# Performance work log

Hardware: AMD Instinct MI355X
Metric: run time of the kernel (lower is better)

Reference implementation:

```python
import jax, jax.numpy as jnp
import numpy as np

EPS_COS = 1e-8
EPS_SHARP = 1e-16


def setup_inputs() -> dict:
    key = jax.random.key(0)
    k1, k2, k3, k4 = jax.random.split(key, 4)
    B, H, R, C, M = 512, 512, 2048, 64, 3
    out_dim = 3 * C + 2 * M + 4  # 202
    h = jax.random.normal(k1, (B, H), dtype=jnp.float32)
    prev_w = jax.random.uniform(k2, (B, R), dtype=jnp.float32)
    prev_w = prev_w / prev_w.sum(axis=1, keepdims=True)  # valid focus distribution
    memory = jax.random.normal(k3, (B, R, C), dtype=jnp.float32)
    fc_w = jax.random.normal(k4, (out_dim, H), dtype=jnp.float32) * 0.05
    fc_b = jnp.zeros((out_dim,), dtype=jnp.float32)
    return {"h": h, "prev_w": prev_w, "memory": memory, "fc_w": fc_w, "fc_b": fc_b}


def _write_head(h, prev_w, memory, fc_w, fc_b):
    B, R, C = memory.shape
    total = fc_w.shape[0]
    shift_len = total - 3 * C - 3          # 2*max_shift + 1
    m = (shift_len - 1) // 2               # max_shift

    z = h @ fc_w.T + fc_b                  # [B, total]
    sizes = [C, 1, 1, shift_len, 1, C, C]
    offs = np.cumsum([0] + sizes)
    k     = jnp.tanh(z[:, offs[0]:offs[1]])                 # [B, C]
    beta  = jax.nn.softplus(z[:, offs[1]:offs[2]])          # [B, 1]
    g     = jax.nn.sigmoid(z[:, offs[2]:offs[3]])           # [B, 1]
    s     = jax.nn.softmax(z[:, offs[3]:offs[4]], axis=1)   # [B, 2m+1]
    gamma = jax.nn.softplus(z[:, offs[4]:offs[5]]) + 1.0    # [B, 1]
    e     = jax.nn.sigmoid(z[:, offs[5]:offs[6]])           # [B, C]
    a     = jnp.tanh(z[:, offs[6]:offs[7]])                 # [B, C]

    # content addressing: cosine similarity of k vs each memory row
    num = jnp.einsum('bc,brc->br', k, memory)
    k_n = jnp.maximum(jnp.linalg.norm(k, axis=1, keepdims=True), EPS_COS)   # [B,1]
    m_n = jnp.maximum(jnp.linalg.norm(memory, axis=2), EPS_COS)             # [B,R]
    w_c = jax.nn.softmax(beta * (num / (k_n * m_n)), axis=1)                # [B,R]

    # gated interpolation
    w_g = g * w_c + (1.0 - g) * prev_w                                      # [B,R]

    # circular shift (per-sample cross-correlation, O(B*R*(2m+1)))
    unrolled = jnp.concatenate([w_g[:, -m:], w_g, w_g[:, :m]], axis=1)      # [B, R+2m]
    windows = jnp.stack([unrolled[:, j:j + R] for j in range(2 * m + 1)], axis=1)  # [B,2m+1,R]
    w_s = jnp.einsum('bjr,bj->br', windows, s)                              # [B,R]

    # sharpen
    w_p = jnp.power(w_s, gamma)
    w = w_p / (w_p.sum(axis=1, keepdims=True) + EPS_SHARP)                  # [B,R]

    # erase + write (fused)
    wE = w[:, :, None]                                                      # [B,R,1]
    new_mem = memory * (1.0 - wE * e[:, None, :]) + wE * a[:, None, :]      # [B,R,C]
    return w, new_mem


def reference(h, prev_w, memory, fc_w, fc_b):
    return _write_head(h, prev_w, memory, fc_w, fc_b)
```

## Files before the change

kernel.cpp:

```cpp
#include <hip/hip_runtime.h>
#include <math.h>

#define BB 512
#define HH 512
#define RR 2048
#define CC 64
#define OUTD 202
#define PSTRIDE 208
#define K_OFF 0
#define E_OFF 64
#define A_OFF 128
#define S_OFF 192
#define COMBO_OFF 199
#define G_OFF 200
#define GAMMA_OFF 201

typedef float f32x4 __attribute__((ext_vector_type(4)));

__device__ __forceinline__ float softplusf_(float x) {
    return (x > 20.f) ? x : log1pf(expf(x));
}
__device__ __forceinline__ float sigmoidf_(float x) {
    return 1.f / (1.f + expf(-x));
}

__global__ __launch_bounds__(256) void params_kernel(
    const float* __restrict__ h, const float* __restrict__ fc_w,
    const float* __restrict__ fc_b, float* __restrict__ pw)
{
    __shared__ float h_sh[8][HH];
    __shared__ float z_sh[8][204];
    const int tid = threadIdx.x;
    const int b0 = blockIdx.x * 8;

    for (int idx = tid; idx < 8 * HH; idx += 256) {
        int j = idx >> 9, i = idx & 511;
        h_sh[j][i] = h[(size_t)(b0 + j) * HH + i];
    }
    __syncthreads();

    if (tid < OUTD) {
        float acc[8];
        #pragma unroll
        for (int j = 0; j < 8; ++j) acc[j] = 0.f;
        const float4* wr4 = (const float4*)(fc_w + (size_t)tid * HH);
        for (int i4 = 0; i4 < HH / 4; ++i4) {
            float4 wv = wr4[i4];
            int i = i4 * 4;
            #pragma unroll
            for (int j = 0; j < 8; ++j) {
                acc[j] = fmaf(wv.x, h_sh[j][i + 0], acc[j]);
                acc[j] = fmaf(wv.y, h_sh[j][i + 1], acc[j]);
                acc[j] = fmaf(wv.z, h_sh[j][i + 2], acc[j]);
                acc[j] = fmaf(wv.w, h_sh[j][i + 3], acc[j]);
            }
        }
        float bias = fc_b[tid];
        #pragma unroll
        for (int j = 0; j < 8; ++j) z_sh[j][tid] = acc[j] + bias;
    }
    __syncthreads();

    for (int idx = tid; idx < 8 * OUTD; idx += 256) {
        int j = idx / OUTD;
        int t = idx - j * OUTD;
        float z = z_sh[j][t];
        float* p = pw + (size_t)(b0 + j) * PSTRIDE;
        if (t < 64)            p[K_OFF + t] = tanhf(z);
        else if (t == 65)      p[G_OFF] = sigmoidf_(z);
        else if (t == 73)      p[GAMMA_OFF] = softplusf_(z) + 1.f;
        else if (t >= 74 && t < 138) p[E_OFF + (t - 74)] = sigmoidf_(z);
        else if (t >= 138)     p[A_OFF + (t - 138)] = tanhf(z);
    }
    __syncthreads();

    if (tid < 8) {
        int j = tid;
        float* p = pw + (size_t)(b0 + j) * PSTRIDE;
        float ss = 0.f;
        for (int c = 0; c < 64; ++c) {
            float kv = tanhf(z_sh[j][c]);
            ss += kv * kv;
        }
        float kn = fmaxf(sqrtf(ss), 1e-8f);
        float beta = softplusf_(z_sh[j][64]);
        p[COMBO_OFF] = beta / kn;
        float mx = -1e30f;
        for (int q = 0; q < 7; ++q) mx = fmaxf(mx, z_sh[j][66 + q]);
        float ev[7], se = 0.f;
        for (int q = 0; q < 7; ++q) { ev[q] = expf(z_sh[j][66 + q] - mx); se += ev[q]; }
        float inv = 1.f / se;
        for (int q = 0; q < 7; ++q) p[S_OFF + q] = ev[q] * inv;
    }
}

__global__ __launch_bounds__(256) void score_kernel(
    const float* __restrict__ memory, const float* __restrict__ pw,
    float* __restrict__ sc)
{
    const int tid = threadIdx.x;
    const int b = blockIdx.x >> 2;
    const int rbase = (blockIdx.x & 3) * 512;
    const int lane16 = tid & 15;
    const int rgrp = tid >> 4;
    const float* p = pw + (size_t)b * PSTRIDE;
    const float4 k4 = *(const float4*)(p + K_OFF + lane16 * 4);
    const float combo = p[COMBO_OFF];
    const float* memb = memory + (size_t)b * RR * CC;

    #pragma unroll 8
    for (int i = 0; i < 32; ++i) {
        int r = rbase + i * 16 + rgrp;
        float4 m4 = *(const float4*)(memb + (size_t)r * CC + lane16 * 4);
        float num = m4.x * k4.x + m4.y * k4.y + m4.z * k4.z + m4.w * k4.w;
        float ssq = m4.x * m4.x + m4.y * m4.y + m4.z * m4.z + m4.w * m4.w;
        #pragma unroll
        for (int m = 1; m < 16; m <<= 1) {
            num += __shfl_xor(num, m, 64);
            ssq += __shfl_xor(ssq, m, 64);
        }
        if (lane16 == 0) {
            float mn = fmaxf(sqrtf(ssq), 1e-8f);
            sc[(size_t)b * RR + r] = __expf(combo * num / mn);
        }
    }
}

__device__ __forceinline__ float block_reduce_sum256(float v, float* red) {
    #pragma unroll
    for (int m = 1; m < 64; m <<= 1) v += __shfl_xor(v, m, 64);
    int wid = threadIdx.x >> 6;
    if ((threadIdx.x & 63) == 0) red[wid] = v;
    __syncthreads();
    float x = red[0] + red[1] + red[2] + red[3];
    __syncthreads();
    return x;
}

__global__ __launch_bounds__(256) void weight_kernel(
    const float* __restrict__ sc, const float* __restrict__ prev_w,
    const float* __restrict__ pw, float* __restrict__ out_w)
{
    __shared__ float buf[RR];
    __shared__ float wg[RR];
    __shared__ float red[4];
    const int b = blockIdx.x;
    const int tid = threadIdx.x;
    const float* p = pw + (size_t)b * PSTRIDE;
    const float g = p[G_OFF];
    const float gamma = p[GAMMA_OFF];
    const float s0 = p[S_OFF + 0], s1 = p[S_OFF + 1], s2 = p[S_OFF + 2],
                s3 = p[S_OFF + 3], s4 = p[S_OFF + 4], s5 = p[S_OFF + 5],
                s6 = p[S_OFF + 6];

    float ls = 0.f;
    for (int r = tid; r < RR; r += 256) {
        float ev = sc[(size_t)b * RR + r];
        buf[r] = ev;
        ls += ev;
    }
    const float se = block_reduce_sum256(ls, red);
    const float invse = 1.f / se;

    for (int r = tid; r < RR; r += 256) {
        wg[r] = g * (buf[r] * invse) + (1.f - g) * prev_w[(size_t)b * RR + r];
    }
    __syncthreads();

    float lp = 0.f;
    for (int r = tid; r < RR; r += 256) {
        float acc = s0 * wg[(r - 3) & (RR - 1)]
                  + s1 * wg[(r - 2) & (RR - 1)]
                  + s2 * wg[(r - 1) & (RR - 1)]
                  + s3 * wg[r]
                  + s4 * wg[(r + 1) & (RR - 1)]
                  + s5 * wg[(r + 2) & (RR - 1)]
                  + s6 * wg[(r + 3) & (RR - 1)];
        float wp = __powf(acc, gamma);
        buf[r] = wp;
        lp += wp;
    }
    const float ps = block_reduce_sum256(lp, red);
    const float invp = 1.f / (ps + 1e-16f);

    for (int r = tid; r < RR; r += 256) {
        out_w[(size_t)b * RR + r] = buf[r] * invp;
    }
}

__global__ __launch_bounds__(256) void update_kernel(
    const float* __restrict__ memory, const float* __restrict__ w,
    const float* __restrict__ pw, float* __restrict__ out_mem)
{
    const int bid = (int)gridDim.x - 1 - (int)blockIdx.x;
    const int b = bid >> 2;
    const int rbase = (bid & 3) * 512;
    const int tid = threadIdx.x;
    const int lane16 = tid & 15;
    const int rgrp = tid >> 4;
    const float* p = pw + (size_t)b * PSTRIDE;
    const f32x4 e4 = *(const f32x4*)(p + E_OFF + lane16 * 4);
    const f32x4 a4 = *(const f32x4*)(p + A_OFF + lane16 * 4);
    const float* memb = memory + (size_t)b * RR * CC;
    float* omb = out_mem + (size_t)b * RR * CC;
    const float* wb = w + (size_t)b * RR;

    #pragma unroll 8
    for (int i = 0; i < 32; ++i) {
        int r = rbase + i * 16 + rgrp;
        float wv = wb[r];
        const f32x4* mp = (const f32x4*)(memb + (size_t)r * CC) + lane16;
        f32x4 m4 = __builtin_nontemporal_load(mp);
        f32x4 o;
        o.x = m4.x * (1.f - wv * e4.x) + wv * a4.x;
        o.y = m4.y * (1.f - wv * e4.y) + wv * a4.y;
        o.z = m4.z * (1.f - wv * e4.z) + wv * a4.z;
        o.w = m4.w * (1.f - wv * e4.w) + wv * a4.w;
        __builtin_nontemporal_store(o, (f32x4*)(omb + (size_t)r * CC) + lane16);
    }
}

extern "C" void kernel_launch(void* const* d_in, const int* in_sizes, int n_in,
                              void* d_out, int out_size, void* d_ws, size_t ws_size,
                              hipStream_t stream) {
    const float* h      = (const float*)d_in[0];
    const float* prev_w = (const float*)d_in[1];
    const float* memory = (const float*)d_in[2];
    const float* fc_w   = (const float*)d_in[3];
    const float* fc_b   = (const float*)d_in[4];

    float* pw      = (float*)d_ws;
    float* out_w   = (float*)d_out;
    float* out_mem = out_w + (size_t)BB * RR;
    float* sc      = out_mem;

    params_kernel<<<64, 256, 0, stream>>>(h, fc_w, fc_b, pw);
    score_kernel<<<BB * 4, 256, 0, stream>>>(memory, pw, sc);
    weight_kernel<<<BB, 256, 0, stream>>>(sc, prev_w, pw, out_w);
    update_kernel<<<BB * 4, 256, 0, stream>>>(memory, out_w, pw, out_mem);
}
```

Measured before the change: 199.1 us.

## Fuse weight normalization and memory update into one 1024-thread kernel per batch

Merges the weight computation and the erase/write memory update into a single kernel with one 1024-thread block per batch row. The final weights stay in shared memory for the update instead of being re-read from global, and one launch is removed. Scores now live in workspace rather than aliasing the output, with the old three-kernel path kept as a fallback when workspace is too small. The trade-off is that the 512 MB-scale memory update now runs on only 512 blocks, which may cut the parallelism available for the bandwidth-bound stream.

```diff
diff --git a/kernel.cpp b/kernel.cpp
--- a/kernel.cpp
+++ b/kernel.cpp
@@ -126,25 +126,34 @@
     }
 }
 
-__device__ __forceinline__ float block_reduce_sum256(float v, float* red) {
+__device__ __forceinline__ float block_reduce_sum16(float v, float* red) {
     #pragma unroll
     for (int m = 1; m < 64; m <<= 1) v += __shfl_xor(v, m, 64);
     int wid = threadIdx.x >> 6;
     if ((threadIdx.x & 63) == 0) red[wid] = v;
     __syncthreads();
-    float x = red[0] + red[1] + red[2] + red[3];
-    __syncthreads();
-    return x;
-}
-
-__global__ __launch_bounds__(256) void weight_kernel(
-    const float* __restrict__ sc, const float* __restrict__ prev_w,
-    const float* __restrict__ pw, float* __restrict__ out_w)
+    if (threadIdx.x < 16) {
+        float x = red[threadIdx.x];
+        #pragma unroll
+        for (int m = 1; m < 16; m <<= 1) x += __shfl_xor(x, m, 64);
+        if (threadIdx.x == 0) red[0] = x;
+    }
+    __syncthreads();
+    float r = red[0];
+    __syncthreads();
+    return r;
+}
+
+__global__ __launch_bounds__(1024) void weight_update_kernel(
+    const float* __restrict__ memory, const float* __restrict__ sc,
+    const float* __restrict__ prev_w, const float* __restrict__ pw,
+    float* __restrict__ out_w, float* __restrict__ out_mem)
 {
     __shared__ float buf[RR];
     __shared__ float wg[RR];
-    __shared__ float red[4];
-    const int b = blockIdx.x;
+    __shared__ float red[16];
+
+    const int b = (int)gridDim.x - 1 - (int)blockIdx.x;
     const int tid = threadIdx.x;
     const float* p = pw + (size_t)b * PSTRIDE;
     const float g = p[G_OFF];
@@ -154,12 +163,98 @@
                 s6 = p[S_OFF + 6];
 
     float ls = 0.f;
+    for (int r = tid; r < RR; r += 1024) {
+        float ev = sc[(size_t)b * RR + r];
+        buf[r] = ev;
+        ls += ev;
+    }
+    const float se = block_reduce_sum16(ls, red);
+    const float invse = 1.f / se;
+
+    for (int r = tid; r < RR; r += 1024) {
+        wg[r] = g * (buf[r] * invse) + (1.f - g) * prev_w[(size_t)b * RR + r];
+    }
+    __syncthreads();
+
+    float lp = 0.f;
+    for (int r = tid; r < RR; r += 1024) {
+        float acc = s0 * wg[(r - 3) & (RR - 1)]
+                  + s1 * wg[(r - 2) & (RR - 1)]
+                  + s2 * wg[(r - 1) & (RR - 1)]
+                  + s3 * wg[r]
+                  + s4 * wg[(r + 1) & (RR - 1)]
+                  + s5 * wg[(r + 2) & (RR - 1)]
+                  + s6 * wg[(r + 3) & (RR - 1)];
+        float wp = __powf(acc, gamma);
+        buf[r] = wp;
+        lp += wp;
+    }
+    const float ps = block_reduce_sum16(lp, red);
+    const float invp = 1.f / (ps + 1e-16f);
+
+    for (int r = tid; r < RR; r += 1024) {
+        float wv = buf[r] * invp;
+        wg[r] = wv;
+        __builtin_nontemporal_store(wv, out_w + (size_t)b * RR + r);
+    }
+    __syncthreads();
+
+    const int lane16 = tid & 15;
+    const int rgrp = tid >> 4;
+    const f32x4 e4 = *(const f32x4*)(p + E_OFF + lane16 * 4);
+    const f32x4 a4 = *(const f32x4*)(p + A_OFF + lane16 * 4);
+    const float* memb = memory + (size_t)b * RR * CC;
+    float* omb = out_mem + (size_t)b * RR * CC;
+
+    #pragma unroll 8
+    for (int i = 0; i < 32; ++i) {
+        int r = i * 64 + rgrp;
+        float wv = wg[r];
+        f32x4 m4 = __builtin_nontemporal_load(
+            (const f32x4*)(memb + (size_t)r * CC) + lane16);
+        f32x4 o;
+        o.x = m4.x * (1.f - wv * e4.x) + wv * a4.x;
+        o.y = m4.y * (1.f - wv * e4.y) + wv * a4.y;
+        o.z = m4.z * (1.f - wv * e4.z) + wv * a4.z;
+        o.w = m4.w * (1.f - wv * e4.w) + wv * a4.w;
+        __builtin_nontemporal_store(o, (f32x4*)(omb + (size_t)r * CC) + lane16);
+    }
+}
+
+__device__ __forceinline__ float block_reduce_sum4(float v, float* red) {
+    #pragma unroll
+    for (int m = 1; m < 64; m <<= 1) v += __shfl_xor(v, m, 64);
+    int wid = threadIdx.x >> 6;
+    if ((threadIdx.x & 63) == 0) red[wid] = v;
+    __syncthreads();
+    float x = red[0] + red[1] + red[2] + red[3];
+    __syncthreads();
+    return x;
+}
+
+__global__ __launch_bounds__(256) void weight_kernel(
+    const float* __restrict__ sc, const float* __restrict__ prev_w,
+    const float* __restrict__ pw, float* __restrict__ out_w)
+{
+    __shared__ float buf[RR];
+    __shared__ float wg[RR];
+    __shared__ float red[4];
+    const int b = blockIdx.x;
+    const int tid = threadIdx.x;
+    const float* p = pw + (size_t)b * PSTRIDE;
+    const float g = p[G_OFF];
+    const float gamma = p[GAMMA_OFF];
+    const float s0 = p[S_OFF + 0], s1 = p[S_OFF + 1], s2 = p[S_OFF + 2],
+                s3 = p[S_OFF + 3], s4 = p[S_OFF + 4], s5 = p[S_OFF + 5],
+                s6 = p[S_OFF + 6];
+
+    float ls = 0.f;
     for (int r = tid; r < RR; r += 256) {
         float ev = sc[(size_t)b * RR + r];
         buf[r] = ev;
         ls += ev;
     }
-    const float se = block_reduce_sum256(ls, red);
+    const float se = block_reduce_sum4(ls, red);
     const float invse = 1.f / se;
 
     for (int r = tid; r < RR; r += 256) {
@@ -180,7 +275,7 @@
         buf[r] = wp;
         lp += wp;
     }
-    const float ps = block_reduce_sum256(lp, red);
+    const float ps = block_reduce_sum4(lp, red);
     const float invp = 1.f / (ps + 1e-16f);
 
     for (int r = tid; r < RR; r += 256) {
@@ -209,8 +304,8 @@
     for (int i = 0; i < 32; ++i) {
         int r = rbase + i * 16 + rgrp;
         float wv = wb[r];
-        const f32x4* mp = (const f32x4*)(memb + (size_t)r * CC) + lane16;
-        f32x4 m4 = __builtin_nontemporal_load(mp);
+        f32x4 m4 = __builtin_nontemporal_load(
+            (const f32x4*)(memb + (size_t)r * CC) + lane16);
         f32x4 o;
         o.x = m4.x * (1.f - wv * e4.x) + wv * a4.x;
         o.y = m4.y * (1.f - wv * e4.y) + wv * a4.y;
@@ -232,10 +327,21 @@
     float* pw      = (float*)d_ws;
     float* out_w   = (float*)d_out;
     float* out_mem = out_w + (size_t)BB * RR;
-    float* sc      = out_mem;
+
+    const size_t pw_bytes = (size_t)BB * PSTRIDE * sizeof(float);
+    const size_t sc_bytes = (size_t)BB * RR * sizeof(float);
 
     params_kernel<<<64, 256, 0, stream>>>(h, fc_w, fc_b, pw);
-    score_kernel<<<BB * 4, 256, 0, stream>>>(memory, pw, sc);
-    weight_kernel<<<BB, 256, 0, stream>>>(sc, prev_w, pw, out_w);
-    update_kernel<<<BB * 4, 256, 0, stream>>>(memory, out_w, pw, out_mem);
-}
+
+    if (ws_size >= pw_bytes + sc_bytes) {
+        float* sc = pw + (size_t)BB * PSTRIDE;
+        score_kernel<<<BB * 4, 256, 0, stream>>>(memory, pw, sc);
+        weight_update_kernel<<<BB, 1024, 0, stream>>>(
+            memory, sc, prev_w, pw, out_w, out_mem);
+    } else {
+        float* sc = out_mem;
+        score_kernel<<<BB * 4, 256, 0, stream>>>(memory, pw, sc);
+        weight_kernel<<<BB, 256, 0, stream>>>(sc, prev_w, pw, out_w);
+        update_kernel<<<BB * 4, 256, 0, stream>>>(memory, out_w, pw, out_mem);
+    }
+}
```

After: 193.5 us. 1.03x faster.

## Chunk score/weight/update pipeline over batch halves for cache reuse of memory

Applied to the files above, without the earlier changes.

Splits the score, weight and update kernels into two batch chunks launched in sequence, and keeps the score buffer in workspace instead of the output. Each chunk's slice of the memory tensor is read by score and then again by update soon after, so the second read can hit the last-level cache instead of HBM. It adds kernel launches, drops the previous reverse block ordering in update, and falls back to the old path if the workspace is too small.

```diff
diff --git a/kernel.cpp b/kernel.cpp
--- a/kernel.cpp
+++ b/kernel.cpp
@@ -14,6 +14,9 @@
 #define COMBO_OFF 199
 #define G_OFF 200
 #define GAMMA_OFF 201
+
+#define NCHUNK 2
+#define CB (BB / NCHUNK)
 
 typedef float f32x4 __attribute__((ext_vector_type(4)));
 
@@ -96,10 +99,10 @@
 
 __global__ __launch_bounds__(256) void score_kernel(
     const float* __restrict__ memory, const float* __restrict__ pw,
-    float* __restrict__ sc)
-{
-    const int tid = threadIdx.x;
-    const int b = blockIdx.x >> 2;
+    float* __restrict__ sc, int bofs)
+{
+    const int tid = threadIdx.x;
+    const int b = bofs + (blockIdx.x >> 2);
     const int rbase = (blockIdx.x & 3) * 512;
     const int lane16 = tid & 15;
     const int rgrp = tid >> 4;
@@ -126,7 +129,7 @@
     }
 }
 
-__device__ __forceinline__ float block_reduce_sum256(float v, float* red) {
+__device__ __forceinline__ float block_reduce_sum4(float v, float* red) {
     #pragma unroll
     for (int m = 1; m < 64; m <<= 1) v += __shfl_xor(v, m, 64);
     int wid = threadIdx.x >> 6;
@@ -139,12 +142,12 @@
 
 __global__ __launch_bounds__(256) void weight_kernel(
     const float* __restrict__ sc, const float* __restrict__ prev_w,
-    const float* __restrict__ pw, float* __restrict__ out_w)
+    const float* __restrict__ pw, float* __restrict__ out_w, int bofs)
 {
     __shared__ float buf[RR];
     __shared__ float wg[RR];
     __shared__ float red[4];
-    const int b = blockIdx.x;
+    const int b = bofs + blockIdx.x;
     const int tid = threadIdx.x;
     const float* p = pw + (size_t)b * PSTRIDE;
     const float g = p[G_OFF];
@@ -159,7 +162,7 @@
         buf[r] = ev;
         ls += ev;
     }
-    const float se = block_reduce_sum256(ls, red);
+    const float se = block_reduce_sum4(ls, red);
     const float invse = 1.f / se;
 
     for (int r = tid; r < RR; r += 256) {
@@ -180,7 +183,7 @@
         buf[r] = wp;
         lp += wp;
     }
-    const float ps = block_reduce_sum256(lp, red);
+    const float ps = block_reduce_sum4(lp, red);
     const float invp = 1.f / (ps + 1e-16f);
 
     for (int r = tid; r < RR; r += 256) {
@@ -190,11 +193,10 @@
 
 __global__ __launch_bounds__(256) void update_kernel(
     const float* __restrict__ memory, const float* __restrict__ w,
-    const float* __restrict__ pw, float* __restrict__ out_mem)
-{
-    const int bid = (int)gridDim.x - 1 - (int)blockIdx.x;
-    const int b = bid >> 2;
-    const int rbase = (bid & 3) * 512;
+    const float* __restrict__ pw, float* __restrict__ out_mem, int bofs)
+{
+    const int b = bofs + ((int)blockIdx.x >> 2);
+    const int rbase = ((int)blockIdx.x & 3) * 512;
     const int tid = threadIdx.x;
     const int lane16 = tid & 15;
     const int rgrp = tid >> 4;
@@ -209,8 +211,8 @@
     for (int i = 0; i < 32; ++i) {
         int r = rbase + i * 16 + rgrp;
         float wv = wb[r];
-        const f32x4* mp = (const f32x4*)(memb + (size_t)r * CC) + lane16;
-        f32x4 m4 = __builtin_nontemporal_load(mp);
+        f32x4 m4 = __builtin_nontemporal_load(
+            (const f32x4*)(memb + (size_t)r * CC) + lane16);
         f32x4 o;
         o.x = m4.x * (1.f - wv * e4.x) + wv * a4.x;
         o.y = m4.y * (1.f - wv * e4.y) + wv * a4.y;
@@ -232,10 +234,25 @@
     float* pw      = (float*)d_ws;
     float* out_w   = (float*)d_out;
     float* out_mem = out_w + (size_t)BB * RR;
-    float* sc      = out_mem;
+
+    const size_t pw_bytes = (size_t)BB * PSTRIDE * sizeof(float);
+    const size_t sc_bytes = (size_t)BB * RR * sizeof(float);
 
     params_kernel<<<64, 256, 0, stream>>>(h, fc_w, fc_b, pw);
-    score_kernel<<<BB * 4, 256, 0, stream>>>(memory, pw, sc);
-    weight_kernel<<<BB, 256, 0, stream>>>(sc, prev_w, pw, out_w);
-    update_kernel<<<BB * 4, 256, 0, stream>>>(memory, out_w, pw, out_mem);
-}
+
+    if (ws_size >= pw_bytes + sc_bytes) {
+        float* sc = pw + (size_t)BB * PSTRIDE;
+        for (int c = 0; c < NCHUNK; ++c) {
+            int b0 = c * CB;
+            score_kernel<<<CB * 4, 256, 0, stream>>>(memory, pw, sc, b0);
+            weight_kernel<<<CB, 256, 0, stream>>>(sc, prev_w, pw, out_w, b0);
+            update_kernel<<<CB * 4, 256, 0, stream>>>(memory, out_w, pw,
+                                                      out_mem, b0);
+        }
+    } else {
+        float* sc = out_mem;
+        score_kernel<<<BB * 4, 256, 0, stream>>>(memory, pw, sc, 0);
+        weight_kernel<<<BB, 256, 0, stream>>>(sc, prev_w, pw, out_w, 0);
+        update_kernel<<<BB * 4, 256, 0, stream>>>(memory, out_w, pw, out_mem, 0);
+    }
+}
```

Result: slower. 215.8 us (+8.4%).

## Split softmax and shift stage across four blocks per sample via partial sums

Applied to the files above, without the earlier changes.

The score kernel now also emits per-block partial sums of the exponentiated scores. The single-block-per-sample weight kernel is replaced by a four-blocks-per-sample convolution kernel that loads a halo tile, applies the gated interpolation and circular shift, and writes un-normalized sharpened weights plus partial sums. The update kernel then applies the final normalization, writes the output weights and updates memory; its memory read is now a plain load instead of a nontemporal one. This path needs a larger workspace, and the old three-kernel path is kept as a fallback when the workspace is too small.

```diff
diff --git a/kernel.cpp b/kernel.cpp
--- a/kernel.cpp
+++ b/kernel.cpp
@@ -94,10 +94,22 @@
     }
 }
 
+__device__ __forceinline__ float block_reduce_sum4(float v, float* red) {
+    #pragma unroll
+    for (int m = 1; m < 64; m <<= 1) v += __shfl_xor(v, m, 64);
+    int wid = threadIdx.x >> 6;
+    if ((threadIdx.x & 63) == 0) red[wid] = v;
+    __syncthreads();
+    float x = red[0] + red[1] + red[2] + red[3];
+    __syncthreads();
+    return x;
+}
+
 __global__ __launch_bounds__(256) void score_kernel(
     const float* __restrict__ memory, const float* __restrict__ pw,
-    float* __restrict__ sc)
-{
+    float* __restrict__ sc, float* __restrict__ esum)
+{
+    __shared__ float red[4];
     const int tid = threadIdx.x;
     const int b = blockIdx.x >> 2;
     const int rbase = (blockIdx.x & 3) * 512;
@@ -108,6 +120,7 @@
     const float combo = p[COMBO_OFF];
     const float* memb = memory + (size_t)b * RR * CC;
 
+    float lsum = 0.f;
     #pragma unroll 8
     for (int i = 0; i < 32; ++i) {
         int r = rbase + i * 16 + rgrp;
@@ -121,37 +134,107 @@
         }
         if (lane16 == 0) {
             float mn = fmaxf(sqrtf(ssq), 1e-8f);
-            sc[(size_t)b * RR + r] = __expf(combo * num / mn);
+            float ev = __expf(combo * num / mn);
+            sc[(size_t)b * RR + r] = ev;
+            lsum += ev;
         }
     }
-}
-
-__device__ __forceinline__ float block_reduce_sum256(float v, float* red) {
-    #pragma unroll
-    for (int m = 1; m < 64; m <<= 1) v += __shfl_xor(v, m, 64);
-    int wid = threadIdx.x >> 6;
-    if ((threadIdx.x & 63) == 0) red[wid] = v;
-    __syncthreads();
-    float x = red[0] + red[1] + red[2] + red[3];
-    __syncthreads();
-    return x;
-}
-
-__global__ __launch_bounds__(256) void weight_kernel(
+    float bs = block_reduce_sum4(lsum, red);
+    if (tid == 0) esum[blockIdx.x] = bs;
+}
+
+__global__ __launch_bounds__(256) void wconv_kernel(
     const float* __restrict__ sc, const float* __restrict__ prev_w,
-    const float* __restrict__ pw, float* __restrict__ out_w)
-{
-    __shared__ float buf[RR];
-    __shared__ float wg[RR];
+    const float* __restrict__ pw, const float* __restrict__ esum,
+    float* __restrict__ wp, float* __restrict__ psum)
+{
+    __shared__ float wgs[518];
     __shared__ float red[4];
-    const int b = blockIdx.x;
-    const int tid = threadIdx.x;
+    const int tid = threadIdx.x;
+    const int b = blockIdx.x >> 2;
+    const int r0 = (blockIdx.x & 3) * 512;
     const float* p = pw + (size_t)b * PSTRIDE;
     const float g = p[G_OFF];
     const float gamma = p[GAMMA_OFF];
     const float s0 = p[S_OFF + 0], s1 = p[S_OFF + 1], s2 = p[S_OFF + 2],
                 s3 = p[S_OFF + 3], s4 = p[S_OFF + 4], s5 = p[S_OFF + 5],
                 s6 = p[S_OFF + 6];
+    const float* eb = esum + (size_t)b * 4;
+    const float invse = 1.f / (eb[0] + eb[1] + eb[2] + eb[3]);
+    const float gi = g * invse, omg = 1.f - g;
+
+    for (int idx = tid; idx < 518; idx += 256) {
+        int r = (r0 - 3 + idx) & (RR - 1);
+        wgs[idx] = gi * sc[(size_t)b * RR + r]
+                 + omg * prev_w[(size_t)b * RR + r];
+    }
+    __syncthreads();
+
+    float lp = 0.f;
+    #pragma unroll
+    for (int t2 = 0; t2 < 2; ++t2) {
+        int idx = t2 * 256 + tid;
+        float acc = s0 * wgs[idx]     + s1 * wgs[idx + 1]
+                  + s2 * wgs[idx + 2] + s3 * wgs[idx + 3]
+                  + s4 * wgs[idx + 4] + s5 * wgs[idx + 5]
+                  + s6 * wgs[idx + 6];
+        float v = __powf(acc, gamma);
+        wp[(size_t)b * RR + r0 + idx] = v;
+        lp += v;
+    }
+    float bs = block_reduce_sum4(lp, red);
+    if (tid == 0) psum[blockIdx.x] = bs;
+}
+
+__global__ __launch_bounds__(256) void update_kernel(
+    const float* __restrict__ memory, const float* __restrict__ wp,
+    const float* __restrict__ psum, const float* __restrict__ pw,
+    float* __restrict__ out_w, float* __restrict__ out_mem)
+{
+    const int bid = (int)gridDim.x - 1 - (int)blockIdx.x;
+    const int b = bid >> 2;
+    const int rbase = (bid & 3) * 512;
+    const int tid = threadIdx.x;
+    const int lane16 = tid & 15;
+    const int rgrp = tid >> 4;
+    const float* p = pw + (size_t)b * PSTRIDE;
+    const float* pb = psum + (size_t)b * 4;
+    const float invp = 1.f / (pb[0] + pb[1] + pb[2] + pb[3] + 1e-16f);
+    const f32x4 e4 = *(const f32x4*)(p + E_OFF + lane16 * 4);
+    const f32x4 a4 = *(const f32x4*)(p + A_OFF + lane16 * 4);
+    const float* memb = memory + (size_t)b * RR * CC;
+    float* omb = out_mem + (size_t)b * RR * CC;
+
+    #pragma unroll 8
+    for (int i = 0; i < 32; ++i) {
+        int r = rbase + i * 16 + rgrp;
+        float wv = wp[(size_t)b * RR + r] * invp;
+        if (lane16 == 0) out_w[(size_t)b * RR + r] = wv;
+        f32x4 m4 = *((const f32x4*)(memb + (size_t)r * CC) + lane16);
+        f32x4 o;
+        o.x = m4.x * (1.f - wv * e4.x) + wv * a4.x;
+        o.y = m4.y * (1.f - wv * e4.y) + wv * a4.y;
+        o.z = m4.z * (1.f - wv * e4.z) + wv * a4.z;
+        o.w = m4.w * (1.f - wv * e4.w) + wv * a4.w;
+        __builtin_nontemporal_store(o, (f32x4*)(omb + (size_t)r * CC) + lane16);
+    }
+}
+
+__global__ __launch_bounds__(256) void weight_kernel_fb(
+    const float* __restrict__ sc, const float* __restrict__ prev_w,
+    const float* __restrict__ pw, float* __restrict__ out_w)
+{
+    __shared__ float buf[RR];
+    __shared__ float wg[RR];
+    __shared__ float red[4];
+    const int b = blockIdx.x;
+    const int tid = threadIdx.x;
+    const float* p = pw + (size_t)b * PSTRIDE;
+    const float g = p[G_OFF];
+    const float gamma = p[GAMMA_OFF];
+    const float s0 = p[S_OFF + 0], s1 = p[S_OFF + 1], s2 = p[S_OFF + 2],
+                s3 = p[S_OFF + 3], s4 = p[S_OFF + 4], s5 = p[S_OFF + 5],
+                s6 = p[S_OFF + 6];
 
     float ls = 0.f;
     for (int r = tid; r < RR; r += 256) {
@@ -159,36 +242,28 @@
         buf[r] = ev;
         ls += ev;
     }
-    const float se = block_reduce_sum256(ls, red);
+    const float se = block_reduce_sum4(ls, red);
     const float invse = 1.f / se;
-
-    for (int r = tid; r < RR; r += 256) {
+    for (int r = tid; r < RR; r += 256)
         wg[r] = g * (buf[r] * invse) + (1.f - g) * prev_w[(size_t)b * RR + r];
-    }
-    __syncthreads();
-
+    __syncthreads();
     float lp = 0.f;
     for (int r = tid; r < RR; r += 256) {
-        float acc = s0 * wg[(r - 3) & (RR - 1)]
-                  + s1 * wg[(r - 2) & (RR - 1)]
-                  + s2 * wg[(r - 1) & (RR - 1)]
-                  + s3 * wg[r]
-                  + s4 * wg[(r + 1) & (RR - 1)]
-                  + s5 * wg[(r + 2) & (RR - 1)]
+        float acc = s0 * wg[(r - 3) & (RR - 1)] + s1 * wg[(r - 2) & (RR - 1)]
+                  + s2 * wg[(r - 1) & (RR - 1)] + s3 * wg[r]
+                  + s4 * wg[(r + 1) & (RR - 1)] + s5 * wg[(r + 2) & (RR - 1)]
                   + s6 * wg[(r + 3) & (RR - 1)];
-        float wp = __powf(acc, gamma);
-        buf[r] = wp;
-        lp += wp;
-    }
-    const float ps = block_reduce_sum256(lp, red);
+        float v = __powf(acc, gamma);
+        buf[r] = v;
+        lp += v;
+    }
+    const float ps = block_reduce_sum4(lp, red);
     const float invp = 1.f / (ps + 1e-16f);
-
-    for (int r = tid; r < RR; r += 256) {
+    for (int r = tid; r < RR; r += 256)
         out_w[(size_t)b * RR + r] = buf[r] * invp;
-    }
-}
-
-__global__ __launch_bounds__(256) void update_kernel(
+}
+
+__global__ __launch_bounds__(256) void update_kernel_fb(
     const float* __restrict__ memory, const float* __restrict__ w,
     const float* __restrict__ pw, float* __restrict__ out_mem)
 {
@@ -209,8 +284,7 @@
     for (int i = 0; i < 32; ++i) {
         int r = rbase + i * 16 + rgrp;
         float wv = wb[r];
-        const f32x4* mp = (const f32x4*)(memb + (size_t)r * CC) + lane16;
-        f32x4 m4 = __builtin_nontemporal_load(mp);
+        f32x4 m4 = *((const f32x4*)(memb + (size_t)r * CC) + lane16);
         f32x4 o;
         o.x = m4.x * (1.f - wv * e4.x) + wv * a4.x;
         o.y = m4.y * (1.f - wv * e4.y) + wv * a4.y;
@@ -232,10 +306,27 @@
     float* pw      = (float*)d_ws;
     float* out_w   = (float*)d_out;
     float* out_mem = out_w + (size_t)BB * RR;
-    float* sc      = out_mem;
+
+    const size_t pw_f   = (size_t)BB * PSTRIDE;
+    const size_t br_f   = (size_t)BB * RR;
+    const size_t need_f = pw_f + 2 * br_f + 2 * (size_t)BB * 4;
 
     params_kernel<<<64, 256, 0, stream>>>(h, fc_w, fc_b, pw);
-    score_kernel<<<BB * 4, 256, 0, stream>>>(memory, pw, sc);
-    weight_kernel<<<BB, 256, 0, stream>>>(sc, prev_w, pw, out_w);
-    update_kernel<<<BB * 4, 256, 0, stream>>>(memory, out_w, pw, out_mem);
-}
+
+    if (ws_size >= need_f * sizeof(float)) {
+        float* sc   = pw + pw_f;
+        float* wp   = sc + br_f;
+        float* esum = wp + br_f;
+        float* psum = esum + (size_t)BB * 4;
+        score_kernel<<<BB * 4, 256, 0, stream>>>(memory, pw, sc, esum);
+        wconv_kernel<<<BB * 4, 256, 0, stream>>>(sc, prev_w, pw, esum, wp, psum);
+        update_kernel<<<BB * 4, 256, 0, stream>>>(memory, wp, psum, pw,
+                                                  out_w, out_mem);
+    } else {
+        float* sc = out_mem;
+        score_kernel<<<BB * 4, 256, 0, stream>>>(memory, pw, sc,
+                                                 pw + pw_f );
+        weight_kernel_fb<<<BB, 256, 0, stream>>>(sc, prev_w, pw, out_w);
+        update_kernel_fb<<<BB * 4, 256, 0, stream>>>(memory, out_w, pw, out_mem);
+    }
+}
```

Measured after the change: 206.6 us. +3.8%, slower.
